# Performance work log

Measured on AMD Instinct MI355X. Metric: run time of the kernel, lower is better.

## Reference

```python
import jax, jax.numpy as jnp
import numpy as np

N = 3000          # num_sample (nodes)
N_OMICS = 3000    # input feature dims for both omics
ENC1, ENC2, NZ = 256, 128, 64


def _xavier(key, fan_in, fan_out):
    limit = float(np.sqrt(6.0 / (fan_in + fan_out)))
    return jax.random.uniform(key, (fan_in, fan_out), jnp.float32, -limit, limit)


def setup_inputs() -> dict:
    key = jax.random.key(0)
    ks = jax.random.split(key, 20)
    inp = {
        "omics_1": jax.random.normal(ks[0], (N, N_OMICS), jnp.float32),
        "omics_2": jax.random.normal(ks[1], (N, N_OMICS), jnp.float32),
    }
    # random dense adjacency, row-normalized (as a typical normalized graph operator)
    for i, name in enumerate(["adj_feature_omics1", "adj_feature_omics2",
                              "adj_spatial_omics1", "adj_spatial_omics2"]):
        a = jax.random.uniform(ks[2 + i], (N, N), jnp.float32)
        inp[name] = a / jnp.sum(a, axis=1, keepdims=True)
    # GNNLayer weights for the four GAE encoders (xavier uniform, as in reset_parameters)
    dims = [(N_OMICS, ENC1), (ENC1, ENC2), (ENC2, NZ)]
    kidx = 6
    for enc in ["f1", "f2", "s1", "s2"]:
        for li, (fi, fo) in enumerate(dims, start=1):
            inp[f"w_{enc}_{li}"] = _xavier(ks[kidx], fi, fo)
            kidx += 1
    return inp


def _gae_encoder(x, adj, w1, w2, w3):
    # GNNLayer: support = act(x @ W); out = spmm(adj, support). Dropout is identity (eval).
    z = adj @ jnp.tanh(x @ w1)          # [N, ENC1]
    z = adj @ jnp.tanh(z @ w2)          # [N, ENC2]
    z = adj @ (z @ w3)                  # [N, NZ]  (no activation on layer 3)
    adj_hat = jax.nn.sigmoid(z @ z.T)   # [N, N]
    return z, adj_hat


def reference(omics_1, omics_2,
              adj_feature_omics1, adj_feature_omics2,
              adj_spatial_omics1, adj_spatial_omics2,
              w_f1_1, w_f1_2, w_f1_3,
              w_f2_1, w_f2_2, w_f2_3,
              w_s1_1, w_s1_2, w_s1_3,
              w_s2_1, w_s2_2, w_s2_3):
    _, a1 = _gae_encoder(omics_1, adj_feature_omics1, w_f1_1, w_f1_2, w_f1_3)
    _, a2 = _gae_encoder(omics_2, adj_feature_omics2, w_f2_1, w_f2_2, w_f2_3)
    _, a3 = _gae_encoder(omics_1, adj_spatial_omics1, w_s1_1, w_s1_2, w_s1_3)
    _, a4 = _gae_encoder(omics_2, adj_spatial_omics2, w_s2_1, w_s2_2, w_s2_3)
    # stacked reconstructed adjacencies from the four encoders [4, N, N]
    return jnp.stack([a1, a2, a3, a4], axis=0)
```

## Files before the change

kernel.cpp:

```cpp
#include <hip/hip_runtime.h>
#include <stdint.h>
#include <stddef.h>


typedef __attribute__((ext_vector_type(8))) _Float16 half8;
typedef __attribute__((ext_vector_type(4))) float f32x4;

#define PAD 3072
#define MR  3000

static __device__ __forceinline__ void async_cp16(const _Float16* g, _Float16* l) {
    __builtin_amdgcn_global_load_lds((const __attribute__((address_space(1))) void*)g,
                                     (__attribute__((address_space(3))) void*)l, 16, 0, 0);
}

struct PrepArgs {
    const float* Wsrc[12];
    _Float16* Wdst[3];
};

__global__ __launch_bounds__(256) void prep_w(PrepArgs p) {
    __shared__ _Float16 lt[64 * 64];
    const int b = blockIdx.x;
    const int t = threadIdx.x;
    const int enc = b / 204;
    int rem = b - enc * 204;
    const float* src; _Float16* dst; int fi, fo, ldk, kt, rt;
    if (rem < 192) {
        src = p.Wsrc[enc * 3 + 0]; dst = p.Wdst[0] + (size_t)enc * 256 * PAD;
        fi = MR; fo = 256; ldk = PAD; kt = rem >> 2; rt = rem & 3;
    } else if (rem < 200) {
        rem -= 192;
        src = p.Wsrc[enc * 3 + 1]; dst = p.Wdst[1] + (size_t)enc * 128 * 256;
        fi = 256; fo = 128; ldk = 256; kt = rem >> 1; rt = rem & 1;
    } else {
        rem -= 200;
        src = p.Wsrc[enc * 3 + 2]; dst = p.Wdst[2] + (size_t)enc * 128 * 128;
        fi = 128; fo = 64; ldk = 128; kt = rem >> 1; rt = rem & 1;
    }
    const int k0 = kt * 64, r0 = rt * 64;
    {
        const int kr = t >> 2, cc = (t & 3) << 4;
        const int gk = k0 + kr;
        const bool kok = gk < fi;
        #pragma unroll
        for (int j = 0; j < 16; ++j) {
            const int gr = r0 + cc + j;
            const float v = (kok && gr < fo) ? src[(size_t)gk * fo + gr] : 0.f;
            lt[(cc + j) * 64 + kr] = (_Float16)v;
        }
    }
    __syncthreads();
    {
        const int rr = t >> 2, kk = (t & 3) << 4;
        half8 a  = *(half8*)&lt[rr * 64 + kk];
        half8 bb = *(half8*)&lt[rr * 64 + kk + 8];
        _Float16* dp = dst + (size_t)(r0 + rr) * ldk + k0 + kk;
        *(half8*)dp = a;
        *(half8*)(dp + 8) = bb;
    }
}

struct GArgs {
    const _Float16* Aall; size_t aStride; int aMask;
    const _Float16* Ball; size_t bStride; int bMask;
    const float* F32[4];
    void* Call; size_t cStride;
    int M, Ncols, Kp, lda, ldb, ldc, mBound, nBound;
};

template<int ACT, int OMODE, int S, int ASRC, int BSRC>
static __device__ __forceinline__
void gemm_body(const GArgs& ga, int bx, int by, int bz, _Float16* smem)
{
    _Float16* As = smem;
    _Float16* Bs = smem + 8192;

    const int z   = bz;
    const int e   = z / S;
    const int ksl = z - e * S;
    const int Kslice = ga.Kp / S;
    const int kbase  = ksl * Kslice;

    const _Float16* A = ga.Aall + (size_t)(e & ga.aMask) * ga.aStride;
    const _Float16* B = ga.Ball + (size_t)(e & ga.bMask) * ga.bStride;
    const float*    F = ga.F32[e];

    const int tm = bx * 128;
    const int tn = by * 128;
    const int t    = threadIdx.x;
    const int lane = t & 63;
    const int w    = t >> 6;
    const int wm   = (w >> 1) * 64;
    const int wn   = (w & 1) * 64;
    const int lr   = lane & 15;
    const int lg   = lane >> 4;

    f32x4 acc[4][4];
    const f32x4 zero = {0.f, 0.f, 0.f, 0.f};
    #pragma unroll
    for (int i = 0; i < 4; ++i)
        #pragma unroll
        for (int j = 0; j < 4; ++j) acc[i][j] = zero;

    const int nkt = Kslice >> 6;
    for (int kt = 0; kt < nkt; ++kt) {
        const int k0 = kbase + (kt << 6);
        if (!ASRC) {
            #pragma unroll
            for (int i = 0; i < 4; ++i) {
                const int c = t + i * 256;
                const int row = c >> 3, slot = c & 7;
                const int ss = slot ^ (row & 7);
                async_cp16(A + (size_t)(tm + row) * ga.lda + k0 + ss * 8, &As[c * 8]);
            }
        }
        if (!BSRC) {
            #pragma unroll
            for (int i = 0; i < 4; ++i) {
                const int c = t + i * 256;
                const int row = c >> 3, slot = c & 7;
                const int ss = slot ^ (row & 7);
                async_cp16(B + (size_t)(tn + row) * ga.ldb + k0 + ss * 8, &Bs[c * 8]);
            }
        }
        if (ASRC) {
            #pragma unroll
            for (int i = 0; i < 4; ++i) {
                const int c = t + i * 256;
                const int row = c >> 3, g = c & 7;
                const int grow = tm + row;
                const int gcol = k0 + g * 8;
                half8 h;
                if (grow < MR && gcol < MR) {
                    const float* ap = F + (size_t)grow * MR + gcol;
                    f32x4 v0 = *(const f32x4*)ap;
                    f32x4 v1 = *(const f32x4*)(ap + 4);
                    #pragma unroll
                    for (int j = 0; j < 4; ++j) { h[j] = (_Float16)v0[j]; h[4 + j] = (_Float16)v1[j]; }
                } else {
                    #pragma unroll
                    for (int j = 0; j < 8; ++j) h[j] = (_Float16)0.f;
                }
                *(half8*)&As[row * 64 + ((g ^ (row & 7)) << 3)] = h;
            }
        }
        if (BSRC) {
            #pragma unroll
            for (int i = 0; i < 4; ++i) {
                const int c = t + i * 256;
                const int row = c >> 3, g = c & 7;
                const int grow = tn + row;
                const int gcol = k0 + g * 8;
                half8 h;
                if (grow < MR && gcol < MR) {
                    const float* bp = F + (size_t)grow * MR + gcol;
                    f32x4 v0 = *(const f32x4*)bp;
                    f32x4 v1 = *(const f32x4*)(bp + 4);
                    #pragma unroll
                    for (int j = 0; j < 4; ++j) { h[j] = (_Float16)v0[j]; h[4 + j] = (_Float16)v1[j]; }
                } else {
                    #pragma unroll
                    for (int j = 0; j < 8; ++j) h[j] = (_Float16)0.f;
                }
                *(half8*)&Bs[row * 64 + ((g ^ (row & 7)) << 3)] = h;
            }
        }
        __syncthreads();

        #pragma unroll
        for (int ks = 0; ks < 2; ++ks) {
            half8 af[4], bf[4];
            #pragma unroll
            for (int mi = 0; mi < 4; ++mi) {
                const int ra = wm + mi * 16 + lr;
                const int s  = (ks * 4 + lg) ^ (ra & 7);
                af[mi] = *(const half8*)((const char*)As + ra * 128 + s * 16);
            }
            #pragma unroll
            for (int ni = 0; ni < 4; ++ni) {
                const int rb = wn + ni * 16 + lr;
                const int s  = (ks * 4 + lg) ^ (rb & 7);
                bf[ni] = *(const half8*)((const char*)Bs + rb * 128 + s * 16);
            }
            #pragma unroll
            for (int mi = 0; mi < 4; ++mi)
                #pragma unroll
                for (int ni = 0; ni < 4; ++ni)
                    acc[mi][ni] = __builtin_amdgcn_mfma_f32_16x16x32_f16(
                        af[mi], bf[ni], acc[mi][ni], 0, 0, 0);
        }
        __syncthreads();
    }

    if (OMODE == 0) {
        _Float16* C = (_Float16*)ga.Call + (size_t)e * ga.cStride;
        #pragma unroll
        for (int mi = 0; mi < 4; ++mi)
            #pragma unroll
            for (int rr = 0; rr < 4; ++rr) {
                const int m = tm + wm + mi * 16 + lg * 4 + rr;
                #pragma unroll
                for (int ni = 0; ni < 4; ++ni) {
                    const int n = tn + wn + ni * 16 + lr;
                    float x = acc[mi][ni][rr];
                    if (ACT) x = tanhf(x);
                    const bool ok = (m < ga.M) && (n < ga.Ncols);
                    C[(size_t)m * ga.ldc + n] = ok ? (_Float16)x : (_Float16)0.f;
                }
            }
    } else {
        float* Cp = (float*)ga.Call + (size_t)(OMODE == 3 ? z : e) * ga.cStride;
        float* ep = (float*)smem + w * 2048;
        #pragma unroll
        for (int hs = 0; hs < 2; ++hs) {
            __syncthreads();
            #pragma unroll
            for (int mi2 = 0; mi2 < 2; ++mi2)
                #pragma unroll
                for (int ni = 0; ni < 4; ++ni)
                    #pragma unroll
                    for (int rr = 0; rr < 4; ++rr) {
                        const int row = mi2 * 16 + lg * 4 + rr;
                        const int col = ni * 16 + lr;
                        const int sw  = (((row ^ (row >> 2)) & 3) << 4);
                        ep[row * 64 + (col ^ sw)] = acc[hs * 2 + mi2][ni][rr];
                    }
            __syncthreads();
            #pragma unroll
            for (int r2 = 0; r2 < 8; ++r2) {
                const int row = r2 * 4 + (lane >> 4);
                const int c4  = (lane & 15) * 4;
                const int sw  = (((row ^ (row >> 2)) & 3) << 4);
                f32x4 v = *(const f32x4*)&ep[row * 64 + (c4 ^ sw)];
                const int gm = tm + wm + hs * 32 + row;
                const int gn = tn + wn + c4;
                if (gm < ga.mBound && gn < ga.nBound) {
                    if (OMODE == 2) {
                        #pragma unroll
                        for (int j = 0; j < 4; ++j)
                            v[j] = 1.0f / (1.0f + __expf(-v[j]));
                        __builtin_nontemporal_store(v, (f32x4*)&Cp[(size_t)gm * ga.ldc + gn]);
                    } else {
                        *(f32x4*)&Cp[(size_t)gm * ga.ldc + gn] = v;
                    }
                }
            }
        }
    }
}

template<int ACT, int OMODE, int S, int ASRC, int BSRC>
__global__ __launch_bounds__(256, 2)
void gemm_bt(GArgs ga) {
    __shared__ _Float16 smem[16384];
    gemm_body<ACT, OMODE, S, ASRC, BSRC>(ga, blockIdx.x, blockIdx.y, blockIdx.z, smem);
}

template<int ACT, int S>
__global__ __launch_bounds__(256)
void reduce_k(const float* __restrict__ P, _Float16* __restrict__ out, size_t region)
{
    const size_t e    = blockIdx.y;
    const size_t base = (size_t)(blockIdx.x * 256 + threadIdx.x) * 8;
    const float* p0 = P + e * S * region + base;
    f32x4 s0 = {0.f, 0.f, 0.f, 0.f}, s1 = s0;
    #pragma unroll
    for (int s = 0; s < S; ++s) {
        const float* p = p0 + (size_t)s * region;
        s0 += *(const f32x4*)p;
        s1 += *(const f32x4*)(p + 4);
    }
    half8 h;
    #pragma unroll
    for (int j = 0; j < 8; ++j) {
        float x = (j < 4) ? s0[j] : s1[j - 4];
        if (ACT) x = tanhf(x);
        h[j] = (_Float16)x;
    }
    *(half8*)(out + e * region + base) = h;
}

extern "C" void kernel_launch(void* const* d_in, const int* in_sizes, int n_in,
                              void* d_out, int out_size, void* d_ws, size_t ws_size,
                              hipStream_t stream)
{
    const float* X1 = (const float*)d_in[0];
    const float* X2 = (const float*)d_in[1];

    const size_t R1 = 786432;
    const size_t R2 = 393216;

    float* Part = (float*)d_out;

    _Float16* hb = (_Float16*)d_ws;
    size_t off = 0;
    auto alloc = [&](size_t elems) { _Float16* p = hb + off; off += elems; return p; };
    _Float16* T1  = alloc(4 * R1);
    _Float16* Z1  = alloc(4 * R1);
    _Float16* T2  = alloc(4 * R2);
    _Float16* Z2  = alloc(4 * R2);
    _Float16* T3  = alloc(4 * R2);
    _Float16* Z3  = alloc(4 * R2);
    _Float16* W1t = alloc(4ull * 256 * PAD);
    _Float16* W2t = alloc(4ull * 128 * 256);
    _Float16* W3t = alloc(4ull * 128 * 128);

    PrepArgs pa;
    for (int enc = 0; enc < 4; ++enc)
        for (int li = 0; li < 3; ++li)
            pa.Wsrc[enc * 3 + li] = (const float*)d_in[6 + enc * 3 + li];
    pa.Wdst[0] = W1t; pa.Wdst[1] = W2t; pa.Wdst[2] = W3t;
    prep_w<<<dim3(816, 1, 1), 256, 0, stream>>>(pa);

    const int BIG = 1 << 30;

    GArgs g1 = { W1t, (size_t)256 * PAD, 3, nullptr, 0, 0,
                 { X1, X2, X1, X2 },
                 Part, R1, 256, PAD, PAD, PAD, MR, PAD, BIG, BIG };
    gemm_bt<0, 3, 4, 0, 1><<<dim3(2, 24, 16), 256, 0, stream>>>(g1);
    reduce_k<1, 4><<<dim3(384, 4, 1), 256, 0, stream>>>(Part, T1, R1);

    GArgs g2 = { nullptr, 0, 0, T1, R1, 3,
                 { (const float*)d_in[2], (const float*)d_in[3],
                   (const float*)d_in[4], (const float*)d_in[5] },
                 Part, R1, PAD, 256, PAD, MR, PAD, 256, BIG, BIG };
    gemm_bt<0, 3, 4, 1, 0><<<dim3(24, 2, 16), 256, 0, stream>>>(g2);
    reduce_k<0, 4><<<dim3(384, 4, 1), 256, 0, stream>>>(Part, Z1, R1);

    GArgs g3 = { W2t, (size_t)128 * 256, 3, Z1, R1, 3,
                 { nullptr, nullptr, nullptr, nullptr },
                 T2, R2, 128, PAD, 256, 256, 256, PAD, BIG, BIG };
    gemm_bt<1, 0, 1, 0, 0><<<dim3(1, 24, 4), 256, 0, stream>>>(g3);

    GArgs g4 = { nullptr, 0, 0, T2, R2, 3,
                 { (const float*)d_in[2], (const float*)d_in[3],
                   (const float*)d_in[4], (const float*)d_in[5] },
                 Part, R2, PAD, 128, PAD, MR, PAD, 128, BIG, BIG };
    gemm_bt<0, 3, 8, 1, 0><<<dim3(24, 1, 32), 256, 0, stream>>>(g4);
    reduce_k<0, 8><<<dim3(192, 4, 1), 256, 0, stream>>>(Part, Z2, R2);

    GArgs g5 = { W3t, (size_t)128 * 128, 3, Z2, R2, 3,
                 { nullptr, nullptr, nullptr, nullptr },
                 T3, R2, 128, PAD, 128, 128, 128, PAD, BIG, BIG };
    gemm_bt<0, 0, 1, 0, 0><<<dim3(1, 24, 4), 256, 0, stream>>>(g5);

    GArgs g6 = { nullptr, 0, 0, T3, R2, 3,
                 { (const float*)d_in[2], (const float*)d_in[3],
                   (const float*)d_in[4], (const float*)d_in[5] },
                 Part, R2, PAD, 128, PAD, MR, PAD, 128, BIG, BIG };
    gemm_bt<0, 3, 8, 1, 0><<<dim3(24, 1, 32), 256, 0, stream>>>(g6);
    reduce_k<0, 8><<<dim3(192, 4, 1), 256, 0, stream>>>(Part, Z3, R2);

    GArgs g7 = { Z3, R2, 3, Z3, R2, 3,
                 { nullptr, nullptr, nullptr, nullptr },
                 d_out, (size_t)MR * MR, MR, MR, 64, 128, 128, MR, MR, MR };
    gemm_bt<0, 2, 1, 0, 0><<<dim3(24, 24, 4), 256, 0, stream>>>(g7);
}
```

Before: 293.6 us.

## Pre-convert adjacency and omics inputs to padded fp16 once in a prep kernel

After: 275.0 us. 1.07x faster.

```diff
diff --git a/kernel.cpp b/kernel.cpp
--- a/kernel.cpp
+++ b/kernel.cpp
@@ -8,6 +8,7 @@
 
 #define PAD 3072
 #define MR  3000
+#define SQ_STRIDE ((size_t)PAD * PAD)
 
 static __device__ __forceinline__ void async_cp16(const _Float16* g, _Float16* l) {
     __builtin_amdgcn_global_load_lds((const __attribute__((address_space(1))) void*)g,
@@ -15,68 +16,101 @@
 }
 
 struct PrepArgs {
-    const float* Wsrc[12];
-    _Float16* Wdst[3];
+    const float* csrc[6];  _Float16* cdst[6];
+    const float* Wsrc[12]; _Float16* Wdst[3];
 };
 
-__global__ __launch_bounds__(256) void prep_w(PrepArgs p) {
+__global__ __launch_bounds__(256) void prep_all(PrepArgs p) {
     __shared__ _Float16 lt[64 * 64];
     const int b = blockIdx.x;
     const int t = threadIdx.x;
-    const int enc = b / 204;
-    int rem = b - enc * 204;
-    const float* src; _Float16* dst; int fi, fo, ldk, kt, rt;
-    if (rem < 192) {
-        src = p.Wsrc[enc * 3 + 0]; dst = p.Wdst[0] + (size_t)enc * 256 * PAD;
-        fi = MR; fo = 256; ldk = PAD; kt = rem >> 2; rt = rem & 3;
-    } else if (rem < 200) {
-        rem -= 192;
-        src = p.Wsrc[enc * 3 + 1]; dst = p.Wdst[1] + (size_t)enc * 128 * 256;
-        fi = 256; fo = 128; ldk = 256; kt = rem >> 1; rt = rem & 1;
+    if (b < 13824) {
+        const int arr = b / 2304;
+        const int idx = (b - arr * 2304) * 256 + t;
+        const int row = idx / 192;
+        const int c0  = (idx - row * 192) * 16;
+        const float* sp = p.csrc[arr] + (size_t)row * MR + c0;
+        _Float16* d = p.cdst[arr] + (size_t)row * PAD + c0;
+        half8 h0, h1;
+        if (row < MR && c0 + 16 <= MR) {
+            f32x4 v0 = *(const f32x4*)sp;
+            f32x4 v1 = *(const f32x4*)(sp + 4);
+            f32x4 v2 = *(const f32x4*)(sp + 8);
+            f32x4 v3 = *(const f32x4*)(sp + 12);
+            #pragma unroll
+            for (int j = 0; j < 4; ++j) {
+                h0[j] = (_Float16)v0[j]; h0[4 + j] = (_Float16)v1[j];
+                h1[j] = (_Float16)v2[j]; h1[4 + j] = (_Float16)v3[j];
+            }
+        } else if (row < MR && c0 < MR) {
+            #pragma unroll
+            for (int j = 0; j < 8; ++j) {
+                h0[j] = (c0 + j     < MR) ? (_Float16)sp[j]     : (_Float16)0.f;
+                h1[j] = (c0 + 8 + j < MR) ? (_Float16)sp[8 + j] : (_Float16)0.f;
+            }
+        } else {
+            #pragma unroll
+            for (int j = 0; j < 8; ++j) { h0[j] = (_Float16)0.f; h1[j] = (_Float16)0.f; }
+        }
+        *(half8*)d = h0;
+        *(half8*)(d + 8) = h1;
     } else {
-        rem -= 200;
-        src = p.Wsrc[enc * 3 + 2]; dst = p.Wdst[2] + (size_t)enc * 128 * 128;
-        fi = 128; fo = 64; ldk = 128; kt = rem >> 1; rt = rem & 1;
-    }
-    const int k0 = kt * 64, r0 = rt * 64;
-    {
-        const int kr = t >> 2, cc = (t & 3) << 4;
-        const int gk = k0 + kr;
-        const bool kok = gk < fi;
-        #pragma unroll
-        for (int j = 0; j < 16; ++j) {
-            const int gr = r0 + cc + j;
-            const float v = (kok && gr < fo) ? src[(size_t)gk * fo + gr] : 0.f;
-            lt[(cc + j) * 64 + kr] = (_Float16)v;
-        }
-    }
-    __syncthreads();
-    {
-        const int rr = t >> 2, kk = (t & 3) << 4;
-        half8 a  = *(half8*)&lt[rr * 64 + kk];
-        half8 bb = *(half8*)&lt[rr * 64 + kk + 8];
-        _Float16* dp = dst + (size_t)(r0 + rr) * ldk + k0 + kk;
-        *(half8*)dp = a;
-        *(half8*)(dp + 8) = bb;
+        const int b2  = b - 13824;
+        const int enc = b2 / 204;
+        int rem = b2 - enc * 204;
+        const float* src; _Float16* dst; int fi, fo, ldk, kt, rt;
+        if (rem < 192) {
+            src = p.Wsrc[enc * 3 + 0]; dst = p.Wdst[0] + (size_t)enc * 256 * PAD;
+            fi = MR; fo = 256; ldk = PAD; kt = rem >> 2; rt = rem & 3;
+        } else if (rem < 200) {
+            rem -= 192;
+            src = p.Wsrc[enc * 3 + 1]; dst = p.Wdst[1] + (size_t)enc * 128 * 256;
+            fi = 256; fo = 128; ldk = 256; kt = rem >> 1; rt = rem & 1;
+        } else {
+            rem -= 200;
+            src = p.Wsrc[enc * 3 + 2]; dst = p.Wdst[2] + (size_t)enc * 128 * 128;
+            fi = 128; fo = 64; ldk = 128; kt = rem >> 1; rt = rem & 1;
+        }
+        const int k0 = kt * 64, r0 = rt * 64;
+        {
+            const int kr = t >> 2, cc = (t & 3) << 4;
+            const int gk = k0 + kr;
+            const bool kok = gk < fi;
+            #pragma unroll
+            for (int j = 0; j < 16; ++j) {
+                const int gr = r0 + cc + j;
+                const float v = (kok && gr < fo) ? src[(size_t)gk * fo + gr] : 0.f;
+                lt[(cc + j) * 64 + kr] = (_Float16)v;
+            }
+        }
+        __syncthreads();
+        {
+            const int rr = t >> 2, kk = (t & 3) << 4;
+            half8 a  = *(half8*)&lt[rr * 64 + kk];
+            half8 bb = *(half8*)&lt[rr * 64 + kk + 8];
+            _Float16* dp = dst + (size_t)(r0 + rr) * ldk + k0 + kk;
+            *(half8*)dp = a;
+            *(half8*)(dp + 8) = bb;
+        }
     }
 }
 
 struct GArgs {
     const _Float16* Aall; size_t aStride; int aMask;
     const _Float16* Ball; size_t bStride; int bMask;
-    const float* F32[4];
     void* Call; size_t cStride;
     int M, Ncols, Kp, lda, ldb, ldc, mBound, nBound;
 };
 
-template<int ACT, int OMODE, int S, int ASRC, int BSRC>
-static __device__ __forceinline__
-void gemm_body(const GArgs& ga, int bx, int by, int bz, _Float16* smem)
+template<int ACT, int OMODE, int S>
+__global__ __launch_bounds__(256, 3)
+void gemm_bt(GArgs ga)
 {
+    __shared__ _Float16 smem[16384];
     _Float16* As = smem;
     _Float16* Bs = smem + 8192;
 
-    const int z   = bz;
+    const int z   = blockIdx.z;
     const int e   = z / S;
     const int ksl = z - e * S;
     const int Kslice = ga.Kp / S;
@@ -84,10 +118,9 @@
 
     const _Float16* A = ga.Aall + (size_t)(e & ga.aMask) * ga.aStride;
     const _Float16* B = ga.Ball + (size_t)(e & ga.bMask) * ga.bStride;
-    const float*    F = ga.F32[e];
-
-    const int tm = bx * 128;
-    const int tn = by * 128;
+
+    const int tm = blockIdx.x * 128;
+    const int tn = blockIdx.y * 128;
     const int t    = threadIdx.x;
     const int lane = t & 63;
     const int w    = t >> 6;
@@ -106,65 +139,19 @@
     const int nkt = Kslice >> 6;
     for (int kt = 0; kt < nkt; ++kt) {
         const int k0 = kbase + (kt << 6);
-        if (!ASRC) {
-            #pragma unroll
-            for (int i = 0; i < 4; ++i) {
-                const int c = t + i * 256;
-                const int row = c >> 3, slot = c & 7;
-                const int ss = slot ^ (row & 7);
-                async_cp16(A + (size_t)(tm + row) * ga.lda + k0 + ss * 8, &As[c * 8]);
-            }
-        }
-        if (!BSRC) {
-            #pragma unroll
-            for (int i = 0; i < 4; ++i) {
-                const int c = t + i * 256;
-                const int row = c >> 3, slot = c & 7;
-                const int ss = slot ^ (row & 7);
-                async_cp16(B + (size_t)(tn + row) * ga.ldb + k0 + ss * 8, &Bs[c * 8]);
-            }
-        }
-        if (ASRC) {
-            #pragma unroll
-            for (int i = 0; i < 4; ++i) {
-                const int c = t + i * 256;
-                const int row = c >> 3, g = c & 7;
-                const int grow = tm + row;
-                const int gcol = k0 + g * 8;
-                half8 h;
-                if (grow < MR && gcol < MR) {
-                    const float* ap = F + (size_t)grow * MR + gcol;
-                    f32x4 v0 = *(const f32x4*)ap;
-                    f32x4 v1 = *(const f32x4*)(ap + 4);
-                    #pragma unroll
-                    for (int j = 0; j < 4; ++j) { h[j] = (_Float16)v0[j]; h[4 + j] = (_Float16)v1[j]; }
-                } else {
-                    #pragma unroll
-                    for (int j = 0; j < 8; ++j) h[j] = (_Float16)0.f;
-                }
-                *(half8*)&As[row * 64 + ((g ^ (row & 7)) << 3)] = h;
-            }
-        }
-        if (BSRC) {
-            #pragma unroll
-            for (int i = 0; i < 4; ++i) {
-                const int c = t + i * 256;
-                const int row = c >> 3, g = c & 7;
-                const int grow = tn + row;
-                const int gcol = k0 + g * 8;
-                half8 h;
-                if (grow < MR && gcol < MR) {
-                    const float* bp = F + (size_t)grow * MR + gcol;
-                    f32x4 v0 = *(const f32x4*)bp;
-                    f32x4 v1 = *(const f32x4*)(bp + 4);
-                    #pragma unroll
-                    for (int j = 0; j < 4; ++j) { h[j] = (_Float16)v0[j]; h[4 + j] = (_Float16)v1[j]; }
-                } else {
-                    #pragma unroll
-                    for (int j = 0; j < 8; ++j) h[j] = (_Float16)0.f;
-                }
-                *(half8*)&Bs[row * 64 + ((g ^ (row & 7)) << 3)] = h;
-            }
+        #pragma unroll
+        for (int i = 0; i < 4; ++i) {
+            const int c = t + i * 256;
+            const int row = c >> 3, slot = c & 7;
+            const int ss = slot ^ (row & 7);
+            async_cp16(A + (size_t)(tm + row) * ga.lda + k0 + ss * 8, &As[c * 8]);
+        }
+        #pragma unroll
+        for (int i = 0; i < 4; ++i) {
+            const int c = t + i * 256;
+            const int row = c >> 3, slot = c & 7;
+            const int ss = slot ^ (row & 7);
+            async_cp16(B + (size_t)(tn + row) * ga.ldb + k0 + ss * 8, &Bs[c * 8]);
         }
         __syncthreads();
 
@@ -250,13 +237,6 @@
     }
 }
 
-template<int ACT, int OMODE, int S, int ASRC, int BSRC>
-__global__ __launch_bounds__(256, 2)
-void gemm_bt(GArgs ga) {
-    __shared__ _Float16 smem[16384];
-    gemm_body<ACT, OMODE, S, ASRC, BSRC>(ga, blockIdx.x, blockIdx.y, blockIdx.z, smem);
-}
-
 template<int ACT, int S>
 __global__ __launch_bounds__(256)
 void reduce_k(const float* __restrict__ P, _Float16* __restrict__ out, size_t region)
@@ -285,17 +265,16 @@
                               void* d_out, int out_size, void* d_ws, size_t ws_size,
                               hipStream_t stream)
 {
-    const float* X1 = (const float*)d_in[0];
-    const float* X2 = (const float*)d_in[1];
-
     const size_t R1 = 786432;
     const size_t R2 = 393216;
 
-    float* Part = (float*)d_out;
+    _Float16* Adj  = (_Float16*)d_out;
+    float*    Part = (float*)(Adj + 4 * SQ_STRIDE);
 
     _Float16* hb = (_Float16*)d_ws;
     size_t off = 0;
     auto alloc = [&](size_t elems) { _Float16* p = hb + off; off += elems; return p; };
+    _Float16* Xh  = alloc(2 * SQ_STRIDE);
     _Float16* T1  = alloc(4 * R1);
     _Float16* Z1  = alloc(4 * R1);
     _Float16* T2  = alloc(4 * R2);
@@ -307,53 +286,49 @@
     _Float16* W3t = alloc(4ull * 128 * 128);
 
     PrepArgs pa;
+    pa.csrc[0] = (const float*)d_in[0]; pa.cdst[0] = Xh;
+    pa.csrc[1] = (const float*)d_in[1]; pa.cdst[1] = Xh + SQ_STRIDE;
+    for (int i = 0; i < 4; ++i) {
+        pa.csrc[2 + i] = (const float*)d_in[2 + i];
+        pa.cdst[2 + i] = Adj + (size_t)i * SQ_STRIDE;
+    }
     for (int enc = 0; enc < 4; ++enc)
         for (int li = 0; li < 3; ++li)
             pa.Wsrc[enc * 3 + li] = (const float*)d_in[6 + enc * 3 + li];
     pa.Wdst[0] = W1t; pa.Wdst[1] = W2t; pa.Wdst[2] = W3t;
-    prep_w<<<dim3(816, 1, 1), 256, 0, stream>>>(pa);
+    prep_all<<<dim3(14640, 1, 1), 256, 0, stream>>>(pa);
 
     const int BIG = 1 << 30;
 
-    GArgs g1 = { W1t, (size_t)256 * PAD, 3, nullptr, 0, 0,
-                 { X1, X2, X1, X2 },
-                 Part, R1, 256, PAD, PAD, PAD, MR, PAD, BIG, BIG };
-    gemm_bt<0, 3, 4, 0, 1><<<dim3(2, 24, 16), 256, 0, stream>>>(g1);
+    GArgs g1 = { W1t, (size_t)256 * PAD, 3, Xh, SQ_STRIDE, 1,
+                 Part, R1, 256, PAD, PAD, PAD, PAD, PAD, BIG, BIG };
+    gemm_bt<0, 3, 4><<<dim3(2, 24, 16), 256, 0, stream>>>(g1);
     reduce_k<1, 4><<<dim3(384, 4, 1), 256, 0, stream>>>(Part, T1, R1);
 
-    GArgs g2 = { nullptr, 0, 0, T1, R1, 3,
-                 { (const float*)d_in[2], (const float*)d_in[3],
-                   (const float*)d_in[4], (const float*)d_in[5] },
-                 Part, R1, PAD, 256, PAD, MR, PAD, 256, BIG, BIG };
-    gemm_bt<0, 3, 4, 1, 0><<<dim3(24, 2, 16), 256, 0, stream>>>(g2);
+    GArgs g2 = { Adj, SQ_STRIDE, 3, T1, R1, 3,
+                 Part, R1, PAD, 256, PAD, PAD, PAD, 256, BIG, BIG };
+    gemm_bt<0, 3, 4><<<dim3(24, 2, 16), 256, 0, stream>>>(g2);
     reduce_k<0, 4><<<dim3(384, 4, 1), 256, 0, stream>>>(Part, Z1, R1);
 
     GArgs g3 = { W2t, (size_t)128 * 256, 3, Z1, R1, 3,
-                 { nullptr, nullptr, nullptr, nullptr },
                  T2, R2, 128, PAD, 256, 256, 256, PAD, BIG, BIG };
-    gemm_bt<1, 0, 1, 0, 0><<<dim3(1, 24, 4), 256, 0, stream>>>(g3);
-
-    GArgs g4 = { nullptr, 0, 0, T2, R2, 3,
-                 { (const float*)d_in[2], (const float*)d_in[3],
-                   (const float*)d_in[4], (const float*)d_in[5] },
-                 Part, R2, PAD, 128, PAD, MR, PAD, 128, BIG, BIG };
-    gemm_bt<0, 3, 8, 1, 0><<<dim3(24, 1, 32), 256, 0, stream>>>(g4);
+    gemm_bt<1, 0, 1><<<dim3(1, 24, 4), 256, 0, stream>>>(g3);
+
+    GArgs g4 = { Adj, SQ_STRIDE, 3, T2, R2, 3,
+                 Part, R2, PAD, 128, PAD, PAD, PAD, 128, BIG, BIG };
+    gemm_bt<0, 3, 8><<<dim3(24, 1, 32), 256, 0, stream>>>(g4);
     reduce_k<0, 8><<<dim3(192, 4, 1), 256, 0, stream>>>(Part, Z2, R2);
 
     GArgs g5 = { W3t, (size_t)128 * 128, 3, Z2, R2, 3,
-                 { nullptr, nullptr, nullptr, nullptr },
                  T3, R2, 128, PAD, 128, 128, 128, PAD, BIG, BIG };
-    gemm_bt<0, 0, 1, 0, 0><<<dim3(1, 24, 4), 256, 0, stream>>>(g5);
-
-    GArgs g6 = { nullptr, 0, 0, T3, R2, 3,
-                 { (const float*)d_in[2], (const float*)d_in[3],
-                   (const float*)d_in[4], (const float*)d_in[5] },
-                 Part, R2, PAD, 128, PAD, MR, PAD, 128, BIG, BIG };
-    gemm_bt<0, 3, 8, 1, 0><<<dim3(24, 1, 32), 256, 0, stream>>>(g6);
+    gemm_bt<0, 0, 1><<<dim3(1, 24, 4), 256, 0, stream>>>(g5);
+
+    GArgs g6 = { Adj, SQ_STRIDE, 3, T3, R2, 3,
+                 Part, R2, PAD, 128, PAD, PAD, PAD, 128, BIG, BIG };
+    gemm_bt<0, 3, 8><<<dim3(24, 1, 32), 256, 0, stream>>>(g6);
     reduce_k<0, 8><<<dim3(192, 4, 1), 256, 0, stream>>>(Part, Z3, R2);
 
     GArgs g7 = { Z3, R2, 3, Z3, R2, 3,
-                 { nullptr, nullptr, nullptr, nullptr },
                  d_out, (size_t)MR * MR, MR, MR, 64, 128, 128, MR, MR, MR };
-    gemm_bt<0, 2, 1, 0, 0><<<dim3(24, 24, 4), 256, 0, stream>>>(g7);
-}
+    gemm_bt<0, 2, 1><<<dim3(24, 24, 4), 256, 0, stream>>>(g7);
+}
```
